# Optimization experiments

Measured on AMD Instinct MI355X. Metric: run time of the kernel, lower is better.

Reference implementation:

```python
import jax, jax.numpy as jnp
import numpy as np

B, K, C, G = 8192, 4096, 4096, 32
EPS = 1e-5


def setup_inputs() -> dict:
    key = jax.random.key(0)
    ks = jax.random.split(key, 4)
    x = jax.random.normal(ks[0], (B, K), dtype=jnp.float32)
    weight = jax.random.normal(ks[1], (C, K), dtype=jnp.float32) * (1.0 / np.sqrt(K))
    bias = jax.random.normal(ks[2], (C,), dtype=jnp.float32) * 0.02
    gn_weight = jnp.ones((C,), dtype=jnp.float32)
    gn_bias = jnp.zeros((C,), dtype=jnp.float32)
    multiply_weight = jax.random.normal(ks[3], (C,), dtype=jnp.float32)
    return {"x": x, "weight": weight, "bias": bias, "gn_weight": gn_weight,
            "gn_bias": gn_bias, "multiply_weight": multiply_weight}


def reference(x, weight, bias, gn_weight, gn_bias, multiply_weight):
    # Linear: y = x @ W^T + b   -> [B, C]
    h = jnp.einsum('bk,ck->bc', x, weight) + bias
    # GroupNorm over each group of C//G channels, per sample
    hg = h.reshape(B, G, C // G)
    mean = jnp.mean(hg, axis=-1, keepdims=True)
    var = jnp.mean(jnp.square(hg), axis=-1, keepdims=True) - jnp.square(mean)
    hn = ((hg - mean) * jax.lax.rsqrt(var + EPS)).reshape(B, C)
    hn = hn * gn_weight + gn_bias
    # Swish -> * multiply_weight -> Swish
    x1 = hn * jax.nn.sigmoid(hn)
    x2 = x1 * multiply_weight
    return x2 * jax.nn.sigmoid(x2)
```

## Files before the change

kernel.cpp:

```cpp
#include <hip/hip_runtime.h>


typedef short bf16x8 __attribute__((ext_vector_type(8)));
typedef unsigned short u16x8 __attribute__((ext_vector_type(8)));
typedef unsigned short u16x4 __attribute__((ext_vector_type(4)));
typedef float fx4 __attribute__((ext_vector_type(4)));

__device__ __forceinline__ unsigned short f2bf(float f) {
    union { float f; unsigned u; } v; v.f = f;
    unsigned r = v.u + 0x7FFFu + ((v.u >> 16) & 1u);
    return (unsigned short)(r >> 16);
}

__device__ __forceinline__ void load_lds16(const void* g, void* l) {
    __builtin_amdgcn_global_load_lds(
        (const __attribute__((address_space(1))) void*)g,
        (__attribute__((address_space(3))) void*)l, 16, 0, 0);
}

__global__ void __launch_bounds__(256)
cvt_both(const float* __restrict__ X, const float* __restrict__ W,
         unsigned short* __restrict__ Xb, unsigned short* __restrict__ Wb,
         long long nX, long long nW) {
    long long i = ((long long)blockIdx.x * 256 + threadIdx.x) * 8;
    const float* src; unsigned short* dst; long long j;
    if (i < nX) { src = X; dst = Xb; j = i; }
    else { j = i - nX; if (j >= nW) return; src = W; dst = Wb; }
    float4 a = *(const float4*)(src + j);
    float4 b = *(const float4*)(src + j + 4);
    u16x8 o;
    o[0] = f2bf(a.x); o[1] = f2bf(a.y); o[2] = f2bf(a.z); o[3] = f2bf(a.w);
    o[4] = f2bf(b.x); o[5] = f2bf(b.y); o[6] = f2bf(b.z); o[7] = f2bf(b.w);
    *(u16x8*)(dst + j) = o;
}

#define BAR()    do { __builtin_amdgcn_s_barrier(); asm volatile("" ::: "memory"); } while (0)
#define LGKM0()  asm volatile("s_waitcnt lgkmcnt(0)" ::: "memory")
#define VMCNT(n) asm volatile("s_waitcnt vmcnt(" #n ")" ::: "memory")

__global__ void __launch_bounds__(512, 2)
gemm256(const unsigned short* __restrict__ X,
        const unsigned short* __restrict__ Wt,
        const float* __restrict__ bias, const float* __restrict__ gnw,
        const float* __restrict__ gnb,  const float* __restrict__ mw,
        float* __restrict__ out)
{
    constexpr int Kd = 4096;
    constexpr int NT = 64;
    __shared__ __align__(16) unsigned short As[32768];
    __shared__ __align__(16) unsigned short Bs[32768];

    const int tid  = threadIdx.x;
    const int w    = tid >> 6;
    const int lane = tid & 63;
    const int wm = w >> 2, wn = w & 3;
    const int lrow = lane & 15, q = lane >> 4;

    const int bid = blockIdx.x;
    const int swz = (bid & 7) * 64 + (bid >> 3);
    const int n0 = (swz & 15) * 256;
    const int m0 = (swz >> 4) * 256;

    const unsigned short* Atile = X  + (size_t)m0 * Kd;
    const unsigned short* Btile = Wt + (size_t)n0 * Kd;

    const int srow0 = w * 16 + (lane >> 2);
    const int skc   = (lane & 3) ^ ((srow0 >> 1) & 3);
    const size_t soff0 = (size_t)srow0 * Kd + skc * 8;
    const size_t soff1 = soff0 + (size_t)128 * Kd;

    const int fsw  = q ^ ((lrow >> 1) & 3);
    const int aoff = (wm * 128 + lrow) * 32 + fsw * 8;
    const int boff = (wn * 64  + lrow) * 32 + fsw * 8;

    fx4 acc[8][4];
    const fx4 zero = {0.f, 0.f, 0.f, 0.f};
    #pragma unroll
    for (int i = 0; i < 8; i++)
        #pragma unroll
        for (int j = 0; j < 4; j++) acc[i][j] = zero;

    bf16x8 fa[4], fb[4];

#define STAGE(gt, reg) do { \
    load_lds16((gt) + soff0, (reg) + w * 512); \
    load_lds16((gt) + soff1, (reg) + 4096 + w * 512); \
} while (0)

#define LDA4(regbase, MH) do { \
    _Pragma("unroll") \
    for (int _i = 0; _i < 4; _i++) \
        fa[_i] = *(const bf16x8*)((regbase) + aoff + (MH) * 2048 + _i * 512); \
} while (0)

#define LDB4(regbase) do { \
    _Pragma("unroll") \
    for (int _j = 0; _j < 4; _j++) \
        fb[_j] = *(const bf16x8*)((regbase) + boff + _j * 512); \
} while (0)

#define MMA(MH) do { \
    __builtin_amdgcn_s_setprio(1); \
    _Pragma("unroll") \
    for (int _i = 0; _i < 4; _i++) \
        _Pragma("unroll") \
        for (int _j = 0; _j < 4; _j++) \
            acc[(MH)*4+_i][_j] = __builtin_amdgcn_mfma_f32_16x16x32_bf16( \
                fa[_i], fb[_j], acc[(MH)*4+_i][_j], 0, 0, 0); \
    __builtin_amdgcn_s_setprio(0); \
} while (0)

#define KTILE(BUF, ktv) do { \
    unsigned short* A0  = As + (BUF) * 16384; \
    unsigned short* A1  = A0 + 8192; \
    unsigned short* B0  = Bs + (BUF) * 16384; \
    unsigned short* B1  = B0 + 8192; \
    unsigned short* nA1 = As + ((BUF) ^ 1) * 16384 + 8192; \
    unsigned short* nB1 = Bs + ((BUF) ^ 1) * 16384 + 8192; \
    int _j1 = (ktv) + 1; if (_j1 > NT - 1) _j1 = NT - 1; \
    int _j2 = (ktv) + 2; if (_j2 > NT - 1) _j2 = NT - 1; \
     \
    LDB4(B0); LDA4(A0, 0); \
    STAGE(Atile + _j1 * 64 + 32, nA1); \
    BAR(); LGKM0(); MMA(0); BAR(); \
     \
    LDA4(A0, 1); \
    STAGE(Btile + _j1 * 64 + 32, nB1); \
    BAR(); LGKM0(); MMA(1); BAR(); \
     \
    LDB4(B1); LDA4(A1, 0); \
    STAGE(Atile + _j2 * 64, A0); \
    BAR(); LGKM0(); MMA(0); BAR(); \
     \
    LDA4(A1, 1); \
    STAGE(Btile + _j2 * 64, B0); \
    BAR(); LGKM0(); MMA(1); \
    VMCNT(4); BAR(); \
} while (0)

    STAGE(Atile + 0,  As + 0);
    STAGE(Btile + 0,  Bs + 0);
    STAGE(Atile + 32, As + 8192);
    STAGE(Btile + 32, Bs + 8192);
    STAGE(Atile + 64, As + 16384);
    STAGE(Btile + 64, Bs + 16384);
    VMCNT(4); BAR();

    #pragma unroll 1
    for (int kt = 0; kt < NT; kt += 2) {
        KTILE(0, kt);
        KTILE(1, kt + 1);
    }

    VMCNT(0); BAR();

    float* redS = (float*)As;
    float* redQ = (float*)As + 1024;

    float bia[4], gwv[4], gbv[4], mwv[4]; int cdx[4];
    #pragma unroll
    for (int nt = 0; nt < 4; nt++) {
        int c = n0 + wn * 64 + nt * 16 + lrow;
        cdx[nt] = c;
        bia[nt] = bias[c]; gwv[nt] = gnw[c]; gbv[nt] = gnb[c]; mwv[nt] = mw[c];
    }
    #pragma unroll
    for (int mt = 0; mt < 8; mt++)
        #pragma unroll
        for (int nt = 0; nt < 4; nt++)
            #pragma unroll
            for (int r = 0; r < 4; r++)
                acc[mt][nt][r] += bia[nt];

    #pragma unroll
    for (int mt = 0; mt < 8; mt++) {
        float sv[4], qv[4];
        #pragma unroll
        for (int r = 0; r < 4; r++) {
            float a = 0.f, b = 0.f;
            #pragma unroll
            for (int nt = 0; nt < 4; nt++) { float v = acc[mt][nt][r]; a += v; b += v * v; }
            sv[r] = a; qv[r] = b;
        }
        #pragma unroll
        for (int off = 1; off < 16; off <<= 1)
            #pragma unroll
            for (int r = 0; r < 4; r++) {
                sv[r] += __shfl_xor(sv[r], off, 64);
                qv[r] += __shfl_xor(qv[r], off, 64);
            }
        if (lrow == 0) {
            #pragma unroll
            for (int r = 0; r < 4; r++) {
                redS[w * 128 + mt * 16 + q * 4 + r] = sv[r];
                redQ[w * 128 + mt * 16 + q * 4 + r] = qv[r];
            }
        }
    }
    __syncthreads();

    const int pw = w ^ 1;
    #pragma unroll
    for (int mt = 0; mt < 8; mt++) {
        #pragma unroll
        for (int r = 0; r < 4; r++) {
            int ri = mt * 16 + q * 4 + r;
            float tot = redS[w * 128 + ri] + redS[pw * 128 + ri];
            float tq  = redQ[w * 128 + ri] + redQ[pw * 128 + ri];
            float mean = tot * (1.0f / 128.0f);
            float rstd = rsqrtf(tq * (1.0f / 128.0f) - mean * mean + 1e-5f);
            size_t row = (size_t)(m0 + wm * 128 + mt * 16 + q * 4 + r);
            float* orow = out + row * 4096;
            #pragma unroll
            for (int nt = 0; nt < 4; nt++) {
                float h  = acc[mt][nt][r];
                float hn = (h - mean) * rstd;
                hn = hn * gwv[nt] + gbv[nt];
                float x1 = hn / (1.0f + __expf(-hn));
                float x2 = x1 * mwv[nt];
                orow[cdx[nt]] = x2 / (1.0f + __expf(-x2));
            }
        }
    }
#undef STAGE
#undef LDA4
#undef LDB4
#undef MMA
#undef KTILE
}

__device__ __forceinline__ void
epilogue_f(fx4 (&acc)[4][4],
           const float* __restrict__ bias, const float* __restrict__ gnw,
           const float* __restrict__ gnb,  const float* __restrict__ mw,
           float* __restrict__ out, int m0, int n0,
           int wm, int wn, int lrow, int q,
           float (*redS)[128], float (*redQ)[128]) {
    constexpr int C = 4096;
    float bia[4], gw[4], gb[4], mwv[4];
    int cidx[4];
    #pragma unroll
    for (int nt = 0; nt < 4; nt++) {
        int c = n0 + wn * 64 + nt * 16 + lrow;
        cidx[nt] = c;
        bia[nt] = bias[c]; gw[nt] = gnw[c]; gb[nt] = gnb[c]; mwv[nt] = mw[c];
    }
    #pragma unroll
    for (int mt = 0; mt < 4; mt++)
        #pragma unroll
        for (int nt = 0; nt < 4; nt++)
            #pragma unroll
            for (int r = 0; r < 4; r++)
                acc[mt][nt][r] += bia[nt];

    float s[4][4], ss[4][4];
    #pragma unroll
    for (int mt = 0; mt < 4; mt++)
        #pragma unroll
        for (int r = 0; r < 4; r++) {
            float a = 0.f, b = 0.f;
            #pragma unroll
            for (int nt = 0; nt < 4; nt++) {
                float v = acc[mt][nt][r];
                a += v; b += v * v;
            }
            s[mt][r] = a; ss[mt][r] = b;
        }
    #pragma unroll
    for (int off = 1; off < 16; off <<= 1)
        #pragma unroll
        for (int mt = 0; mt < 4; mt++)
            #pragma unroll
            for (int r = 0; r < 4; r++) {
                s[mt][r]  += __shfl_xor(s[mt][r],  off, 64);
                ss[mt][r] += __shfl_xor(ss[mt][r], off, 64);
            }
    if (lrow == 0) {
        #pragma unroll
        for (int mt = 0; mt < 4; mt++)
            #pragma unroll
            for (int r = 0; r < 4; r++) {
                int row = wm * 64 + mt * 16 + q * 4 + r;
                redS[wn][row] = s[mt][r];
                redQ[wn][row] = ss[mt][r];
            }
    }
    __syncthreads();

    #pragma unroll
    for (int mt = 0; mt < 4; mt++)
        #pragma unroll
        for (int r = 0; r < 4; r++) {
            int row = wm * 64 + mt * 16 + q * 4 + r;
            float tot  = redS[0][row] + redS[1][row];
            float tq   = redQ[0][row] + redQ[1][row];
            float mean = tot * (1.0f / 128.0f);
            float var  = tq * (1.0f / 128.0f) - mean * mean;
            s[mt][r]  = mean;
            ss[mt][r] = rsqrtf(var + 1e-5f);
        }

    #pragma unroll
    for (int mt = 0; mt < 4; mt++)
        #pragma unroll
        for (int r = 0; r < 4; r++) {
            size_t row = (size_t)(m0 + wm * 64 + mt * 16 + q * 4 + r);
            #pragma unroll
            for (int nt = 0; nt < 4; nt++) {
                float h  = acc[mt][nt][r];
                float hn = (h - s[mt][r]) * ss[mt][r];
                hn = hn * gw[nt] + gb[nt];
                float x1 = hn / (1.0f + __expf(-hn));
                float x2 = x1 * mwv[nt];
                float y  = x2 / (1.0f + __expf(-x2));
                out[row * (size_t)C + cidx[nt]] = y;
            }
        }
}

__global__ void __launch_bounds__(256)
gemm_f32cvt(const float* __restrict__ X, const float* __restrict__ Wt,
            const float* __restrict__ bias, const float* __restrict__ gnw,
            const float* __restrict__ gnb,  const float* __restrict__ mw,
            float* __restrict__ out)
{
    constexpr int K = 4096;
    __shared__ __align__(16) unsigned short As[128 * 32];
    __shared__ __align__(16) unsigned short Bs[128 * 32];
    __shared__ float redS[2][128];
    __shared__ float redQ[2][128];

    const int tid  = threadIdx.x;
    const int wave = tid >> 6;
    const int lane = tid & 63;
    const int wm = wave >> 1, wn = wave & 1;
    const int lrow = lane & 15;
    const int q    = lane >> 4;

    const int m0 = blockIdx.y * 128;
    const int n0 = blockIdx.x * 128;

    const int srow = tid >> 3;
    const int sk   = (tid & 7) * 4;

    fx4 acc[4][4];
    const fx4 zero = {0.f, 0.f, 0.f, 0.f};
    #pragma unroll
    for (int i = 0; i < 4; i++)
        #pragma unroll
        for (int j = 0; j < 4; j++) acc[i][j] = zero;

    for (int k0 = 0; k0 < K; k0 += 32) {
        #pragma unroll
        for (int j = 0; j < 4; j++) {
            int row = j * 32 + srow;
            float4 va = *(const float4*)(X  + (size_t)(m0 + row) * K + k0 + sk);
            float4 vb = *(const float4*)(Wt + (size_t)(n0 + row) * K + k0 + sk);
            u16x4 oa = { f2bf(va.x), f2bf(va.y), f2bf(va.z), f2bf(va.w) };
            u16x4 ob = { f2bf(vb.x), f2bf(vb.y), f2bf(vb.z), f2bf(vb.w) };
            *(u16x4*)&As[row * 32 + sk] = oa;
            *(u16x4*)&Bs[row * 32 + sk] = ob;
        }
        __syncthreads();

        bf16x8 af[4], bfr[4];
        #pragma unroll
        for (int mt = 0; mt < 4; mt++)
            af[mt] = *(const bf16x8*)&As[(wm * 64 + mt * 16 + lrow) * 32 + q * 8];
        #pragma unroll
        for (int nt = 0; nt < 4; nt++)
            bfr[nt] = *(const bf16x8*)&Bs[(wn * 64 + nt * 16 + lrow) * 32 + q * 8];

        #pragma unroll
        for (int mt = 0; mt < 4; mt++)
            #pragma unroll
            for (int nt = 0; nt < 4; nt++)
                acc[mt][nt] = __builtin_amdgcn_mfma_f32_16x16x32_bf16(
                    af[mt], bfr[nt], acc[mt][nt], 0, 0, 0);
        __syncthreads();
    }

    epilogue_f(acc, bias, gnw, gnb, mw, out, m0, n0, wm, wn, lrow, q, redS, redQ);
}

extern "C" void kernel_launch(void* const* d_in, const int* in_sizes, int n_in,
                              void* d_out, int out_size, void* d_ws, size_t ws_size,
                              hipStream_t stream) {
    (void)in_sizes; (void)n_in; (void)out_size;
    const float* X    = (const float*)d_in[0];
    const float* Wt   = (const float*)d_in[1];
    const float* bias = (const float*)d_in[2];
    const float* gnw  = (const float*)d_in[3];
    const float* gnb  = (const float*)d_in[4];
    const float* mw   = (const float*)d_in[5];
    float* out = (float*)d_out;

    const long long nX = 8192LL * 4096LL;
    const long long nW = 4096LL * 4096LL;
    const size_t need = (size_t)(nX + nW) * 2;

    if (ws_size >= need) {
        unsigned short* Xb = (unsigned short*)d_ws;
        unsigned short* Wb = Xb + nX;
        cvt_both<<<(int)((nX + nW) / 8 / 256), 256, 0, stream>>>(X, Wt, Xb, Wb, nX, nW);
        gemm256<<<512, 512, 0, stream>>>(Xb, Wb, bias, gnw, gnb, mw, out);
    } else {
        dim3 grid(4096 / 128, 8192 / 128);
        gemm_f32cvt<<<grid, 256, 0, stream>>>(X, Wt, bias, gnw, gnb, mw, out);
    }
}
```

Baseline: 540.7 us.

## Double-buffer MFMA fragments to overlap LDS reads with matrix math

Register fragments for A and B are now double-buffered, so the next sub-step's LDS reads are issued before the current MFMA block runs. The explicit lgkmcnt(0) waits and about half of the barriers are dropped, and the vmcnt thresholds are retuned to match the new staging order. The goal is to hide LDS read latency behind MFMA work. In exchange it adds register pressure under launch_bounds(512,2) and relies on subtle barrier and waitcnt correctness, so a race could surface.

```diff
diff --git a/kernel.cpp b/kernel.cpp
--- a/kernel.cpp
+++ b/kernel.cpp
@@ -35,7 +35,6 @@
 }
 
 #define BAR()    do { __builtin_amdgcn_s_barrier(); asm volatile("" ::: "memory"); } while (0)
-#define LGKM0()  asm volatile("s_waitcnt lgkmcnt(0)" ::: "memory")
 #define VMCNT(n) asm volatile("s_waitcnt vmcnt(" #n ")" ::: "memory")
 
 __global__ void __launch_bounds__(512, 2)
@@ -80,33 +79,33 @@
         #pragma unroll
         for (int j = 0; j < 4; j++) acc[i][j] = zero;
 
-    bf16x8 fa[4], fb[4];
+    bf16x8 fa[2][4], fb[2][4];
 
 #define STAGE(gt, reg) do { \
     load_lds16((gt) + soff0, (reg) + w * 512); \
     load_lds16((gt) + soff1, (reg) + 4096 + w * 512); \
 } while (0)
 
-#define LDA4(regbase, MH) do { \
+#define PREF_A(S, base, MH) do { \
     _Pragma("unroll") \
     for (int _i = 0; _i < 4; _i++) \
-        fa[_i] = *(const bf16x8*)((regbase) + aoff + (MH) * 2048 + _i * 512); \
+        fa[S][_i] = *(const bf16x8*)((base) + aoff + (MH) * 2048 + _i * 512); \
 } while (0)
 
-#define LDB4(regbase) do { \
+#define PREF_B(S, base) do { \
     _Pragma("unroll") \
     for (int _j = 0; _j < 4; _j++) \
-        fb[_j] = *(const bf16x8*)((regbase) + boff + _j * 512); \
+        fb[S][_j] = *(const bf16x8*)((base) + boff + _j * 512); \
 } while (0)
 
-#define MMA(MH) do { \
+#define MMA(AS, BS, MH) do { \
     __builtin_amdgcn_s_setprio(1); \
     _Pragma("unroll") \
     for (int _i = 0; _i < 4; _i++) \
         _Pragma("unroll") \
         for (int _j = 0; _j < 4; _j++) \
             acc[(MH)*4+_i][_j] = __builtin_amdgcn_mfma_f32_16x16x32_bf16( \
-                fa[_i], fb[_j], acc[(MH)*4+_i][_j], 0, 0, 0); \
+                fa[AS][_i], fb[BS][_j], acc[(MH)*4+_i][_j], 0, 0, 0); \
     __builtin_amdgcn_s_setprio(0); \
 } while (0)
 
@@ -115,27 +114,34 @@
     unsigned short* A1  = A0 + 8192; \
     unsigned short* B0  = Bs + (BUF) * 16384; \
     unsigned short* B1  = B0 + 8192; \
-    unsigned short* nA1 = As + ((BUF) ^ 1) * 16384 + 8192; \
-    unsigned short* nB1 = Bs + ((BUF) ^ 1) * 16384 + 8192; \
+    unsigned short* nA0 = As + ((BUF) ^ 1) * 16384; \
+    unsigned short* nA1 = nA0 + 8192; \
+    unsigned short* nB0 = Bs + ((BUF) ^ 1) * 16384; \
+    unsigned short* nB1 = nB0 + 8192; \
     int _j1 = (ktv) + 1; if (_j1 > NT - 1) _j1 = NT - 1; \
     int _j2 = (ktv) + 2; if (_j2 > NT - 1) _j2 = NT - 1; \
      \
-    LDB4(B0); LDA4(A0, 0); \
+    BAR(); \
+    PREF_A(1, A0, 1); \
     STAGE(Atile + _j1 * 64 + 32, nA1); \
-    BAR(); LGKM0(); MMA(0); BAR(); \
+    MMA(0, 0, 0); \
      \
-    LDA4(A0, 1); \
+    VMCNT(6); BAR(); \
+    PREF_B(1, B1); \
+    PREF_A(0, A1, 0); \
     STAGE(Btile + _j1 * 64 + 32, nB1); \
-    BAR(); LGKM0(); MMA(1); BAR(); \
+    MMA(1, 0, 1); \
      \
-    LDB4(B1); LDA4(A1, 0); \
+    BAR(); \
+    PREF_A(1, A1, 1); \
     STAGE(Atile + _j2 * 64, A0); \
-    BAR(); LGKM0(); MMA(0); BAR(); \
+    MMA(0, 1, 0); \
      \
-    LDA4(A1, 1); \
+    VMCNT(6); BAR(); \
+    PREF_B(0, nB0); \
+    PREF_A(0, nA0, 0); \
     STAGE(Btile + _j2 * 64, B0); \
-    BAR(); LGKM0(); MMA(1); \
-    VMCNT(4); BAR(); \
+    MMA(1, 1, 1); \
 } while (0)
 
     STAGE(Atile + 0,  As + 0);
@@ -144,7 +150,9 @@
     STAGE(Btile + 32, Bs + 8192);
     STAGE(Atile + 64, As + 16384);
     STAGE(Btile + 64, Bs + 16384);
-    VMCNT(4); BAR();
+    VMCNT(8); BAR();
+    PREF_B(0, Bs);
+    PREF_A(0, As, 0);
 
     #pragma unroll 1
     for (int kt = 0; kt < NT; kt += 2) {
@@ -223,8 +231,8 @@
         }
     }
 #undef STAGE
-#undef LDA4
-#undef LDB4
+#undef PREF_A
+#undef PREF_B
 #undef MMA
 #undef KTILE
 }
```

After: 554.8 us. 2.6% more time.

## Use 4-wave 256x256 GEMM tile with 128x128 per-wave subtiles

Applied to the files above, without the earlier changes.

Replaces the 8-wave block (128x64 per wave) with a 4-wave block where each wave computes a 128x128 subtile, doubling register accumulators and raising MFMA-to-LDS-read ratio. The K-loop is restructured into a two-buffer pipeline with finer vmcnt waits and fewer barriers, interleaving global->LDS staging with MMA groups. Because a wave now owns a full 128-channel group, GroupNorm statistics are reduced with shuffles only, removing the LDS reduction and extra syncthreads. Risks include high VGPR pressure (256 accumulator floats plus fragments) limiting occupancy to one block per CU and less latency hiding.

```diff
diff --git a/kernel.cpp b/kernel.cpp
--- a/kernel.cpp
+++ b/kernel.cpp
@@ -35,15 +35,14 @@
 }
 
 #define BAR()    do { __builtin_amdgcn_s_barrier(); asm volatile("" ::: "memory"); } while (0)
-#define LGKM0()  asm volatile("s_waitcnt lgkmcnt(0)" ::: "memory")
 #define VMCNT(n) asm volatile("s_waitcnt vmcnt(" #n ")" ::: "memory")
 
-__global__ void __launch_bounds__(512, 2)
-gemm256(const unsigned short* __restrict__ X,
-        const unsigned short* __restrict__ Wt,
-        const float* __restrict__ bias, const float* __restrict__ gnw,
-        const float* __restrict__ gnb,  const float* __restrict__ mw,
-        float* __restrict__ out)
+__global__ void __launch_bounds__(256, 1)
+gemm256w4(const unsigned short* __restrict__ X,
+          const unsigned short* __restrict__ Wt,
+          const float* __restrict__ bias, const float* __restrict__ gnw,
+          const float* __restrict__ gnb,  const float* __restrict__ mw,
+          float* __restrict__ out)
 {
     constexpr int Kd = 4096;
     constexpr int NT = 64;
@@ -53,7 +52,7 @@
     const int tid  = threadIdx.x;
     const int w    = tid >> 6;
     const int lane = tid & 63;
-    const int wm = w >> 2, wn = w & 3;
+    const int wm = w >> 1, wn = w & 1;
     const int lrow = lane & 15, q = lane >> 4;
 
     const int bid = blockIdx.x;
@@ -64,155 +63,126 @@
     const unsigned short* Atile = X  + (size_t)m0 * Kd;
     const unsigned short* Btile = Wt + (size_t)n0 * Kd;
 
-    const int srow0 = w * 16 + (lane >> 2);
-    const int skc   = (lane & 3) ^ ((srow0 >> 1) & 3);
-    const size_t soff0 = (size_t)srow0 * Kd + skc * 8;
-    const size_t soff1 = soff0 + (size_t)128 * Kd;
+    const int base_r = w * 16 + (lane >> 2);
+    const int skc    = (lane & 3) ^ ((base_r >> 1) & 3);
+    const size_t soff0 = (size_t)base_r * Kd + skc * 8;
 
     const int fsw  = q ^ ((lrow >> 1) & 3);
     const int aoff = (wm * 128 + lrow) * 32 + fsw * 8;
-    const int boff = (wn * 64  + lrow) * 32 + fsw * 8;
-
-    fx4 acc[8][4];
+    const int boff = (wn * 128 + lrow) * 32 + fsw * 8;
+
+    fx4 acc[8][8];
     const fx4 zero = {0.f, 0.f, 0.f, 0.f};
     #pragma unroll
     for (int i = 0; i < 8; i++)
         #pragma unroll
-        for (int j = 0; j < 4; j++) acc[i][j] = zero;
-
-    bf16x8 fa[4], fb[4];
-
-#define STAGE(gt, reg) do { \
-    load_lds16((gt) + soff0, (reg) + w * 512); \
-    load_lds16((gt) + soff1, (reg) + 4096 + w * 512); \
-} while (0)
-
-#define LDA4(regbase, MH) do { \
+        for (int j = 0; j < 8; j++) acc[i][j] = zero;
+
+    bf16x8 a0[8], a1[8], b0[4], b1[4], b2[4], b3[4];
+
+#define STAGEQ(gsrc, ldsbase) do { \
     _Pragma("unroll") \
-    for (int _i = 0; _i < 4; _i++) \
-        fa[_i] = *(const bf16x8*)((regbase) + aoff + (MH) * 2048 + _i * 512); \
-} while (0)
-
-#define LDB4(regbase) do { \
+    for (int _l = 0; _l < 4; _l++) \
+        load_lds16((gsrc) + soff0 + (size_t)(_l * 64) * Kd, \
+                   (ldsbase) + _l * 2048 + w * 512); \
+} while (0)
+
+#define RD_A(dst, base, KH) do { \
+    _Pragma("unroll") \
+    for (int _i = 0; _i < 8; _i++) \
+        dst[_i] = *(const bf16x8*)((base) + (KH) * 8192 + aoff + _i * 512); \
+} while (0)
+
+#define RD_B(dst, base, KH, NH) do { \
     _Pragma("unroll") \
     for (int _j = 0; _j < 4; _j++) \
-        fb[_j] = *(const bf16x8*)((regbase) + boff + _j * 512); \
-} while (0)
-
-#define MMA(MH) do { \
+        dst[_j] = *(const bf16x8*)((base) + (KH) * 8192 + boff + ((NH) * 4 + _j) * 512); \
+} while (0)
+
+#define MMA(A8, B4, NH) do { \
     __builtin_amdgcn_s_setprio(1); \
     _Pragma("unroll") \
-    for (int _i = 0; _i < 4; _i++) \
+    for (int _i = 0; _i < 8; _i++) \
         _Pragma("unroll") \
         for (int _j = 0; _j < 4; _j++) \
-            acc[(MH)*4+_i][_j] = __builtin_amdgcn_mfma_f32_16x16x32_bf16( \
-                fa[_i], fb[_j], acc[(MH)*4+_i][_j], 0, 0, 0); \
+            acc[_i][(NH) * 4 + _j] = __builtin_amdgcn_mfma_f32_16x16x32_bf16( \
+                A8[_i], B4[_j], acc[_i][(NH) * 4 + _j], 0, 0, 0); \
     __builtin_amdgcn_s_setprio(0); \
 } while (0)
 
-#define KTILE(BUF, ktv) do { \
-    unsigned short* A0  = As + (BUF) * 16384; \
-    unsigned short* A1  = A0 + 8192; \
-    unsigned short* B0  = Bs + (BUF) * 16384; \
-    unsigned short* B1  = B0 + 8192; \
-    unsigned short* nA1 = As + ((BUF) ^ 1) * 16384 + 8192; \
-    unsigned short* nB1 = Bs + ((BUF) ^ 1) * 16384 + 8192; \
+#define KTILE(C, ktv) do { \
+    unsigned short* Ab  = As + (C) * 16384; \
+    unsigned short* Bb  = Bs + (C) * 16384; \
+    unsigned short* nAb = As + ((C) ^ 1) * 16384; \
+    unsigned short* nBb = Bs + ((C) ^ 1) * 16384; \
     int _j1 = (ktv) + 1; if (_j1 > NT - 1) _j1 = NT - 1; \
-    int _j2 = (ktv) + 2; if (_j2 > NT - 1) _j2 = NT - 1; \
-     \
-    LDB4(B0); LDA4(A0, 0); \
-    STAGE(Atile + _j1 * 64 + 32, nA1); \
-    BAR(); LGKM0(); MMA(0); BAR(); \
-     \
-    LDA4(A0, 1); \
-    STAGE(Btile + _j1 * 64 + 32, nB1); \
-    BAR(); LGKM0(); MMA(1); BAR(); \
-     \
-    LDB4(B1); LDA4(A1, 0); \
-    STAGE(Atile + _j2 * 64, A0); \
-    BAR(); LGKM0(); MMA(0); BAR(); \
-     \
-    LDA4(A1, 1); \
-    STAGE(Btile + _j2 * 64, B0); \
-    BAR(); LGKM0(); MMA(1); \
-    VMCNT(4); BAR(); \
-} while (0)
-
-    STAGE(Atile + 0,  As + 0);
-    STAGE(Btile + 0,  Bs + 0);
-    STAGE(Atile + 32, As + 8192);
-    STAGE(Btile + 32, Bs + 8192);
-    STAGE(Atile + 64, As + 16384);
-    STAGE(Btile + 64, Bs + 16384);
-    VMCNT(4); BAR();
+    VMCNT(8); BAR();                        \
+    RD_A(a0, Ab, 0); \
+    RD_B(b0, Bb, 0, 0); \
+    STAGEQ(Atile + _j1 * 64, nAb);          \
+    VMCNT(4); BAR();                        \
+    RD_B(b1, Bb, 0, 1); \
+    RD_A(a1, Ab, 1); \
+    RD_B(b2, Bb, 1, 0); \
+    STAGEQ(Btile + _j1 * 64, nBb);          \
+    MMA(a0, b0, 0);                         \
+    RD_B(b3, Bb, 1, 1); \
+    STAGEQ(Atile + _j1 * 64 + 32, nAb + 8192);   \
+    MMA(a0, b1, 1);                         \
+    STAGEQ(Btile + _j1 * 64 + 32, nBb + 8192);   \
+    MMA(a1, b2, 0);                         \
+    MMA(a1, b3, 1);                         \
+} while (0)
+
+    STAGEQ(Atile + 0,  As + 0);
+    STAGEQ(Btile + 0,  Bs + 0);
+    STAGEQ(Atile + 32, As + 8192);
+    STAGEQ(Btile + 32, Bs + 8192);
+    VMCNT(0); BAR();
 
     #pragma unroll 1
     for (int kt = 0; kt < NT; kt += 2) {
         KTILE(0, kt);
         KTILE(1, kt + 1);
     }
-
-    VMCNT(0); BAR();
-
-    float* redS = (float*)As;
-    float* redQ = (float*)As + 1024;
-
-    float bia[4], gwv[4], gbv[4], mwv[4]; int cdx[4];
-    #pragma unroll
-    for (int nt = 0; nt < 4; nt++) {
-        int c = n0 + wn * 64 + nt * 16 + lrow;
+    VMCNT(0);
+
+    float bia[8], gwv[8], gbv[8], mwv[8]; int cdx[8];
+    #pragma unroll
+    for (int nt = 0; nt < 8; nt++) {
+        int c = n0 + wn * 128 + nt * 16 + lrow;
         cdx[nt] = c;
         bia[nt] = bias[c]; gwv[nt] = gnw[c]; gbv[nt] = gnb[c]; mwv[nt] = mw[c];
     }
     #pragma unroll
     for (int mt = 0; mt < 8; mt++)
         #pragma unroll
-        for (int nt = 0; nt < 4; nt++)
+        for (int nt = 0; nt < 8; nt++)
             #pragma unroll
             for (int r = 0; r < 4; r++)
                 acc[mt][nt][r] += bia[nt];
 
     #pragma unroll
     for (int mt = 0; mt < 8; mt++) {
-        float sv[4], qv[4];
         #pragma unroll
         for (int r = 0; r < 4; r++) {
-            float a = 0.f, b = 0.f;
-            #pragma unroll
-            for (int nt = 0; nt < 4; nt++) { float v = acc[mt][nt][r]; a += v; b += v * v; }
-            sv[r] = a; qv[r] = b;
-        }
-        #pragma unroll
-        for (int off = 1; off < 16; off <<= 1)
-            #pragma unroll
-            for (int r = 0; r < 4; r++) {
-                sv[r] += __shfl_xor(sv[r], off, 64);
-                qv[r] += __shfl_xor(qv[r], off, 64);
-            }
-        if (lrow == 0) {
-            #pragma unroll
-            for (int r = 0; r < 4; r++) {
-                redS[w * 128 + mt * 16 + q * 4 + r] = sv[r];
-                redQ[w * 128 + mt * 16 + q * 4 + r] = qv[r];
-            }
-        }
-    }
-    __syncthreads();
-
-    const int pw = w ^ 1;
-    #pragma unroll
-    for (int mt = 0; mt < 8; mt++) {
-        #pragma unroll
-        for (int r = 0; r < 4; r++) {
-            int ri = mt * 16 + q * 4 + r;
-            float tot = redS[w * 128 + ri] + redS[pw * 128 + ri];
-            float tq  = redQ[w * 128 + ri] + redQ[pw * 128 + ri];
-            float mean = tot * (1.0f / 128.0f);
-            float rstd = rsqrtf(tq * (1.0f / 128.0f) - mean * mean + 1e-5f);
+            float s = 0.f, ss = 0.f;
+            #pragma unroll
+            for (int nt = 0; nt < 8; nt++) {
+                float v = acc[mt][nt][r];
+                s += v; ss += v * v;
+            }
+            #pragma unroll
+            for (int off = 1; off < 16; off <<= 1) {
+                s  += __shfl_xor(s,  off, 64);
+                ss += __shfl_xor(ss, off, 64);
+            }
+            float mean = s * (1.0f / 128.0f);
+            float rstd = rsqrtf(ss * (1.0f / 128.0f) - mean * mean + 1e-5f);
             size_t row = (size_t)(m0 + wm * 128 + mt * 16 + q * 4 + r);
             float* orow = out + row * 4096;
             #pragma unroll
-            for (int nt = 0; nt < 4; nt++) {
+            for (int nt = 0; nt < 8; nt++) {
                 float h  = acc[mt][nt][r];
                 float hn = (h - mean) * rstd;
                 hn = hn * gwv[nt] + gbv[nt];
@@ -222,9 +192,9 @@
             }
         }
     }
-#undef STAGE
-#undef LDA4
-#undef LDB4
+#undef STAGEQ
+#undef RD_A
+#undef RD_B
 #undef MMA
 #undef KTILE
 }
@@ -403,7 +373,7 @@
         unsigned short* Xb = (unsigned short*)d_ws;
         unsigned short* Wb = Xb + nX;
         cvt_both<<<(int)((nX + nW) / 8 / 256), 256, 0, stream>>>(X, Wt, Xb, Wb, nX, nW);
-        gemm256<<<512, 512, 0, stream>>>(Xb, Wb, bias, gnw, gnb, mw, out);
+        gemm256w4<<<512, 256, 0, stream>>>(Xb, Wb, bias, gnw, gnb, mw, out);
     } else {
         dim3 grid(4096 / 128, 8192 / 128);
         gemm_f32cvt<<<grid, 256, 0, stream>>>(X, Wt, bias, gnw, gnb, mw, out);
```

New measurement: 1.047 ms. 1.94x slower.

## Fuse fp32-to-bf16 conversion into GEMM staging, dropping the separate convert pass

Applied to the files above, without the earlier changes.

Removes the standalone conversion kernel and the bf16 workspace copies of X and W. The GEMM now loads fp32 tiles into registers, converts them to packed bf16, and writes them to LDS, pipelined one stage ahead of the MFMA loop. This saves a full read-and-write pass over both inputs. In exchange it gives up async global-to-LDS loads, doubles the global bytes read per tile, and raises register pressure for the staging buffers. The unused fallback kernel is also removed.

```diff
diff --git a/kernel.cpp b/kernel.cpp
--- a/kernel.cpp
+++ b/kernel.cpp
@@ -1,49 +1,26 @@
 #include <hip/hip_runtime.h>
+#include <hip/hip_bf16.h>
 
 
 typedef short bf16x8 __attribute__((ext_vector_type(8)));
-typedef unsigned short u16x8 __attribute__((ext_vector_type(8)));
-typedef unsigned short u16x4 __attribute__((ext_vector_type(4)));
 typedef float fx4 __attribute__((ext_vector_type(4)));
-
-__device__ __forceinline__ unsigned short f2bf(float f) {
-    union { float f; unsigned u; } v; v.f = f;
-    unsigned r = v.u + 0x7FFFu + ((v.u >> 16) & 1u);
-    return (unsigned short)(r >> 16);
+typedef unsigned uint4v __attribute__((ext_vector_type(4)));
+
+__device__ __forceinline__ unsigned pk2(float a, float b) {
+    __hip_bfloat162 h = __float22bfloat162_rn(make_float2(a, b));
+    union { __hip_bfloat162 h; unsigned u; } v; v.h = h;
+    return v.u;
 }
 
-__device__ __forceinline__ void load_lds16(const void* g, void* l) {
-    __builtin_amdgcn_global_load_lds(
-        (const __attribute__((address_space(1))) void*)g,
-        (__attribute__((address_space(3))) void*)l, 16, 0, 0);
-}
-
-__global__ void __launch_bounds__(256)
-cvt_both(const float* __restrict__ X, const float* __restrict__ W,
-         unsigned short* __restrict__ Xb, unsigned short* __restrict__ Wb,
-         long long nX, long long nW) {
-    long long i = ((long long)blockIdx.x * 256 + threadIdx.x) * 8;
-    const float* src; unsigned short* dst; long long j;
-    if (i < nX) { src = X; dst = Xb; j = i; }
-    else { j = i - nX; if (j >= nW) return; src = W; dst = Wb; }
-    float4 a = *(const float4*)(src + j);
-    float4 b = *(const float4*)(src + j + 4);
-    u16x8 o;
-    o[0] = f2bf(a.x); o[1] = f2bf(a.y); o[2] = f2bf(a.z); o[3] = f2bf(a.w);
-    o[4] = f2bf(b.x); o[5] = f2bf(b.y); o[6] = f2bf(b.z); o[7] = f2bf(b.w);
-    *(u16x8*)(dst + j) = o;
-}
-
-#define BAR()    do { __builtin_amdgcn_s_barrier(); asm volatile("" ::: "memory"); } while (0)
-#define LGKM0()  asm volatile("s_waitcnt lgkmcnt(0)" ::: "memory")
-#define VMCNT(n) asm volatile("s_waitcnt vmcnt(" #n ")" ::: "memory")
+#define BAR()   do { __builtin_amdgcn_s_barrier(); asm volatile("" ::: "memory"); } while (0)
+#define LGKM0() asm volatile("s_waitcnt lgkmcnt(0)" ::: "memory")
 
 __global__ void __launch_bounds__(512, 2)
-gemm256(const unsigned short* __restrict__ X,
-        const unsigned short* __restrict__ Wt,
-        const float* __restrict__ bias, const float* __restrict__ gnw,
-        const float* __restrict__ gnb,  const float* __restrict__ mw,
-        float* __restrict__ out)
+gemm256f(const float* __restrict__ X,
+         const float* __restrict__ Wt,
+         const float* __restrict__ bias, const float* __restrict__ gnw,
+         const float* __restrict__ gnb,  const float* __restrict__ mw,
+         float* __restrict__ out)
 {
     constexpr int Kd = 4096;
     constexpr int NT = 64;
@@ -61,13 +38,14 @@
     const int n0 = (swz & 15) * 256;
     const int m0 = (swz >> 4) * 256;
 
-    const unsigned short* Atile = X  + (size_t)m0 * Kd;
-    const unsigned short* Btile = Wt + (size_t)n0 * Kd;
-
-    const int srow0 = w * 16 + (lane >> 2);
-    const int skc   = (lane & 3) ^ ((srow0 >> 1) & 3);
-    const size_t soff0 = (size_t)srow0 * Kd + skc * 8;
-    const size_t soff1 = soff0 + (size_t)128 * Kd;
+    const float* Atile = X  + (size_t)m0 * Kd;
+    const float* Btile = Wt + (size_t)n0 * Kd;
+
+    const int s_r   = tid >> 2;
+    const int s_c   = tid & 3;
+    const int s_swz = s_c ^ ((s_r >> 1) & 3);
+    const size_t goff = (size_t)s_r * Kd + s_c * 8;
+    const int    loff = s_r * 32 + s_swz * 8;
 
     const int fsw  = q ^ ((lrow >> 1) & 3);
     const int aoff = (wm * 128 + lrow) * 32 + fsw * 8;
@@ -81,10 +59,22 @@
         for (int j = 0; j < 4; j++) acc[i][j] = zero;
 
     bf16x8 fa[4], fb[4];
-
-#define STAGE(gt, reg) do { \
-    load_lds16((gt) + soff0, (reg) + w * 512); \
-    load_lds16((gt) + soff1, (reg) + 4096 + w * 512); \
+    float4 s0[4], s1[4], s2[4], s3[4];
+
+#define GLOAD(S, src) do { \
+    S[0] = *(const float4*)((src) + goff); \
+    S[1] = *(const float4*)((src) + goff + 4); \
+    S[2] = *(const float4*)((src) + goff + (size_t)128 * Kd); \
+    S[3] = *(const float4*)((src) + goff + (size_t)128 * Kd + 4); \
+} while (0)
+
+#define DSW(S, region) do { \
+    uint4v _v0 = { pk2(S[0].x, S[0].y), pk2(S[0].z, S[0].w), \
+                   pk2(S[1].x, S[1].y), pk2(S[1].z, S[1].w) }; \
+    uint4v _v1 = { pk2(S[2].x, S[2].y), pk2(S[2].z, S[2].w), \
+                   pk2(S[3].x, S[3].y), pk2(S[3].z, S[3].w) }; \
+    *(uint4v*)((region) + loff) = _v0; \
+    *(uint4v*)((region) + loff + 4096) = _v1; \
 } while (0)
 
 #define LDA4(regbase, MH) do { \
@@ -110,49 +100,56 @@
     __builtin_amdgcn_s_setprio(0); \
 } while (0)
 
-#define KTILE(BUF, ktv) do { \
-    unsigned short* A0  = As + (BUF) * 16384; \
+#define KTILE(C, ktv) do { \
+    unsigned short* A0  = As + (C) * 16384; \
     unsigned short* A1  = A0 + 8192; \
-    unsigned short* B0  = Bs + (BUF) * 16384; \
+    unsigned short* B0  = Bs + (C) * 16384; \
     unsigned short* B1  = B0 + 8192; \
-    unsigned short* nA1 = As + ((BUF) ^ 1) * 16384 + 8192; \
-    unsigned short* nB1 = Bs + ((BUF) ^ 1) * 16384 + 8192; \
+    unsigned short* nA0 = As + ((C) ^ 1) * 16384; \
+    unsigned short* nA1 = nA0 + 8192; \
+    unsigned short* nB0 = Bs + ((C) ^ 1) * 16384; \
+    unsigned short* nB1 = nB0 + 8192; \
     int _j1 = (ktv) + 1; if (_j1 > NT - 1) _j1 = NT - 1; \
     int _j2 = (ktv) + 2; if (_j2 > NT - 1) _j2 = NT - 1; \
      \
     LDB4(B0); LDA4(A0, 0); \
-    STAGE(Atile + _j1 * 64 + 32, nA1); \
+    GLOAD(s0, Atile + _j1 * 64 + 32);    \
+    DSW(s2, nA0);                        \
     BAR(); LGKM0(); MMA(0); BAR(); \
      \
     LDA4(A0, 1); \
-    STAGE(Btile + _j1 * 64 + 32, nB1); \
+    GLOAD(s1, Btile + _j1 * 64 + 32);    \
+    DSW(s3, nB0);                        \
     BAR(); LGKM0(); MMA(1); BAR(); \
      \
     LDB4(B1); LDA4(A1, 0); \
-    STAGE(Atile + _j2 * 64, A0); \
+    GLOAD(s2, Atile + _j2 * 64);         \
+    DSW(s0, nA1);                        \
     BAR(); LGKM0(); MMA(0); BAR(); \
      \
     LDA4(A1, 1); \
-    STAGE(Btile + _j2 * 64, B0); \
-    BAR(); LGKM0(); MMA(1); \
-    VMCNT(4); BAR(); \
-} while (0)
-
-    STAGE(Atile + 0,  As + 0);
-    STAGE(Btile + 0,  Bs + 0);
-    STAGE(Atile + 32, As + 8192);
-    STAGE(Btile + 32, Bs + 8192);
-    STAGE(Atile + 64, As + 16384);
-    STAGE(Btile + 64, Bs + 16384);
-    VMCNT(4); BAR();
+    GLOAD(s3, Btile + _j2 * 64);         \
+    DSW(s1, nB1);                        \
+    BAR(); LGKM0(); MMA(1); BAR(); \
+} while (0)
+
+    GLOAD(s0, Atile + 0);
+    GLOAD(s1, Btile + 0);
+    GLOAD(s2, Atile + 32);
+    GLOAD(s3, Btile + 32);
+    DSW(s0, As + 0);
+    DSW(s1, Bs + 0);
+    DSW(s2, As + 8192);
+    DSW(s3, Bs + 8192);
+    GLOAD(s2, Atile + 64);
+    GLOAD(s3, Btile + 64);
+    LGKM0(); BAR();
 
     #pragma unroll 1
     for (int kt = 0; kt < NT; kt += 2) {
         KTILE(0, kt);
         KTILE(1, kt + 1);
     }
-
-    VMCNT(0); BAR();
 
     float* redS = (float*)As;
     float* redQ = (float*)As + 1024;
@@ -222,171 +219,18 @@
             }
         }
     }
-#undef STAGE
+#undef GLOAD
+#undef DSW
 #undef LDA4
 #undef LDB4
 #undef MMA
 #undef KTILE
 }
 
-__device__ __forceinline__ void
-epilogue_f(fx4 (&acc)[4][4],
-           const float* __restrict__ bias, const float* __restrict__ gnw,
-           const float* __restrict__ gnb,  const float* __restrict__ mw,
-           float* __restrict__ out, int m0, int n0,
-           int wm, int wn, int lrow, int q,
-           float (*redS)[128], float (*redQ)[128]) {
-    constexpr int C = 4096;
-    float bia[4], gw[4], gb[4], mwv[4];
-    int cidx[4];
-    #pragma unroll
-    for (int nt = 0; nt < 4; nt++) {
-        int c = n0 + wn * 64 + nt * 16 + lrow;
-        cidx[nt] = c;
-        bia[nt] = bias[c]; gw[nt] = gnw[c]; gb[nt] = gnb[c]; mwv[nt] = mw[c];
-    }
-    #pragma unroll
-    for (int mt = 0; mt < 4; mt++)
-        #pragma unroll
-        for (int nt = 0; nt < 4; nt++)
-            #pragma unroll
-            for (int r = 0; r < 4; r++)
-                acc[mt][nt][r] += bia[nt];
-
-    float s[4][4], ss[4][4];
-    #pragma unroll
-    for (int mt = 0; mt < 4; mt++)
-        #pragma unroll
-        for (int r = 0; r < 4; r++) {
-            float a = 0.f, b = 0.f;
-            #pragma unroll
-            for (int nt = 0; nt < 4; nt++) {
-                float v = acc[mt][nt][r];
-                a += v; b += v * v;
-            }
-            s[mt][r] = a; ss[mt][r] = b;
-        }
-    #pragma unroll
-    for (int off = 1; off < 16; off <<= 1)
-        #pragma unroll
-        for (int mt = 0; mt < 4; mt++)
-            #pragma unroll
-            for (int r = 0; r < 4; r++) {
-                s[mt][r]  += __shfl_xor(s[mt][r],  off, 64);
-                ss[mt][r] += __shfl_xor(ss[mt][r], off, 64);
-            }
-    if (lrow == 0) {
-        #pragma unroll
-        for (int mt = 0; mt < 4; mt++)
-            #pragma unroll
-            for (int r = 0; r < 4; r++) {
-                int row = wm * 64 + mt * 16 + q * 4 + r;
-                redS[wn][row] = s[mt][r];
-                redQ[wn][row] = ss[mt][r];
-            }
-    }
-    __syncthreads();
-
-    #pragma unroll
-    for (int mt = 0; mt < 4; mt++)
-        #pragma unroll
-        for (int r = 0; r < 4; r++) {
-            int row = wm * 64 + mt * 16 + q * 4 + r;
-            float tot  = redS[0][row] + redS[1][row];
-            float tq   = redQ[0][row] + redQ[1][row];
-            float mean = tot * (1.0f / 128.0f);
-            float var  = tq * (1.0f / 128.0f) - mean * mean;
-            s[mt][r]  = mean;
-            ss[mt][r] = rsqrtf(var + 1e-5f);
-        }
-
-    #pragma unroll
-    for (int mt = 0; mt < 4; mt++)
-        #pragma unroll
-        for (int r = 0; r < 4; r++) {
-            size_t row = (size_t)(m0 + wm * 64 + mt * 16 + q * 4 + r);
-            #pragma unroll
-            for (int nt = 0; nt < 4; nt++) {
-                float h  = acc[mt][nt][r];
-                float hn = (h - s[mt][r]) * ss[mt][r];
-                hn = hn * gw[nt] + gb[nt];
-                float x1 = hn / (1.0f + __expf(-hn));
-                float x2 = x1 * mwv[nt];
-                float y  = x2 / (1.0f + __expf(-x2));
-                out[row * (size_t)C + cidx[nt]] = y;
-            }
-        }
-}
-
-__global__ void __launch_bounds__(256)
-gemm_f32cvt(const float* __restrict__ X, const float* __restrict__ Wt,
-            const float* __restrict__ bias, const float* __restrict__ gnw,
-            const float* __restrict__ gnb,  const float* __restrict__ mw,
-            float* __restrict__ out)
-{
-    constexpr int K = 4096;
-    __shared__ __align__(16) unsigned short As[128 * 32];
-    __shared__ __align__(16) unsigned short Bs[128 * 32];
-    __shared__ float redS[2][128];
-    __shared__ float redQ[2][128];
-
-    const int tid  = threadIdx.x;
-    const int wave = tid >> 6;
-    const int lane = tid & 63;
-    const int wm = wave >> 1, wn = wave & 1;
-    const int lrow = lane & 15;
-    const int q    = lane >> 4;
-
-    const int m0 = blockIdx.y * 128;
-    const int n0 = blockIdx.x * 128;
-
-    const int srow = tid >> 3;
-    const int sk   = (tid & 7) * 4;
-
-    fx4 acc[4][4];
-    const fx4 zero = {0.f, 0.f, 0.f, 0.f};
-    #pragma unroll
-    for (int i = 0; i < 4; i++)
-        #pragma unroll
-        for (int j = 0; j < 4; j++) acc[i][j] = zero;
-
-    for (int k0 = 0; k0 < K; k0 += 32) {
-        #pragma unroll
-        for (int j = 0; j < 4; j++) {
-            int row = j * 32 + srow;
-            float4 va = *(const float4*)(X  + (size_t)(m0 + row) * K + k0 + sk);
-            float4 vb = *(const float4*)(Wt + (size_t)(n0 + row) * K + k0 + sk);
-            u16x4 oa = { f2bf(va.x), f2bf(va.y), f2bf(va.z), f2bf(va.w) };
-            u16x4 ob = { f2bf(vb.x), f2bf(vb.y), f2bf(vb.z), f2bf(vb.w) };
-            *(u16x4*)&As[row * 32 + sk] = oa;
-            *(u16x4*)&Bs[row * 32 + sk] = ob;
-        }
-        __syncthreads();
-
-        bf16x8 af[4], bfr[4];
-        #pragma unroll
-        for (int mt = 0; mt < 4; mt++)
-            af[mt] = *(const bf16x8*)&As[(wm * 64 + mt * 16 + lrow) * 32 + q * 8];
-        #pragma unroll
-        for (int nt = 0; nt < 4; nt++)
-            bfr[nt] = *(const bf16x8*)&Bs[(wn * 64 + nt * 16 + lrow) * 32 + q * 8];
-
-        #pragma unroll
-        for (int mt = 0; mt < 4; mt++)
-            #pragma unroll
-            for (int nt = 0; nt < 4; nt++)
-                acc[mt][nt] = __builtin_amdgcn_mfma_f32_16x16x32_bf16(
-                    af[mt], bfr[nt], acc[mt][nt], 0, 0, 0);
-        __syncthreads();
-    }
-
-    epilogue_f(acc, bias, gnw, gnb, mw, out, m0, n0, wm, wn, lrow, q, redS, redQ);
-}
-
 extern "C" void kernel_launch(void* const* d_in, const int* in_sizes, int n_in,
                               void* d_out, int out_size, void* d_ws, size_t ws_size,
                               hipStream_t stream) {
-    (void)in_sizes; (void)n_in; (void)out_size;
+    (void)in_sizes; (void)n_in; (void)out_size; (void)d_ws; (void)ws_size;
     const float* X    = (const float*)d_in[0];
     const float* Wt   = (const float*)d_in[1];
     const float* bias = (const float*)d_in[2];
@@ -395,17 +239,5 @@
     const float* mw   = (const float*)d_in[5];
     float* out = (float*)d_out;
 
-    const long long nX = 8192LL * 4096LL;
-    const long long nW = 4096LL * 4096LL;
-    const size_t need = (size_t)(nX + nW) * 2;
-
-    if (ws_size >= need) {
-        unsigned short* Xb = (unsigned short*)d_ws;
-        unsigned short* Wb = Xb + nX;
-        cvt_both<<<(int)((nX + nW) / 8 / 256), 256, 0, stream>>>(X, Wt, Xb, Wb, nX, nW);
-        gemm256<<<512, 512, 0, stream>>>(Xb, Wb, bias, gnw, gnb, mw, out);
-    } else {
-        dim3 grid(4096 / 128, 8192 / 128);
-        gemm_f32cvt<<<grid, 256, 0, stream>>>(X, Wt, bias, gnw, gnb, mw, out);
-    }
+    gemm256f<<<512, 512, 0, stream>>>(X, Wt, bias, gnw, gnb, mw, out);
 }
```

New measurement: 740.7 us. +37.0%, slower.
